# Performance work log

Hardware: AMD Instinct MI355X
Metric: run time of the kernel (lower is better)

## Reference

```python
import jax, jax.numpy as jnp
import numpy as np

N, E = 50000, 800000
IN_C, HID_C, OUT_C = 64, 64, 32
K, T = 2, 2  # num_stacks, num_layers (shared_weights=True)


def setup_inputs() -> dict:
    key = jax.random.key(0)
    ks = jax.random.split(key, 11)
    p = lambda k, shape, fan: jax.random.normal(k, shape, jnp.float32) / np.sqrt(fan)
    return {
        "x": jax.random.normal(ks[0], (N, IN_C), jnp.float32),
        "edge_index": jax.random.randint(ks[1], (2, E), 0, N, jnp.int32),
        # ARMAConv 1: in_c -> hid_c
        "init_w1": p(ks[2], (K, IN_C, HID_C), IN_C),
        "w1": p(ks[3], (1, K, HID_C, HID_C), HID_C),
        "root_w1": p(ks[4], (1, K, IN_C, HID_C), IN_C),
        "b1": 0.01 * jax.random.normal(ks[5], (1, K, 1, HID_C), jnp.float32),
        # ARMAConv 2: hid_c -> out_c
        "init_w2": p(ks[6], (K, HID_C, OUT_C), HID_C),
        "w2": p(ks[7], (1, K, OUT_C, OUT_C), OUT_C),
        "root_w2": p(ks[8], (1, K, HID_C, OUT_C), HID_C),
        "b2": 0.01 * jax.random.normal(ks[9], (1, K, 1, OUT_C), jnp.float32),
    }


def _gcn_norm(src, dst, num_nodes):
    # PyG gcn_norm with add_self_loops=False, edge_weight = 1
    deg = jax.ops.segment_sum(jnp.ones(src.shape[0], jnp.float32), dst,
                              num_segments=num_nodes)
    dinv = jnp.where(deg > 0, deg ** -0.5, 0.0)
    return dinv[src] * dinv[dst]  # [E]


def _arma_conv(x, src, dst, norm, init_w, w, root_w, b, num_nodes):
    # x: [N, F_in]; shared weights across layers, act=ReLU, eval mode (no dropout)
    root = jnp.einsum('nf,kfg->nkg', x, root_w[0]) + b[0, :, 0, :]  # [N,K,Fout]
    out = x
    for t in range(T):
        if t == 0:
            out = jnp.einsum('nf,kfg->nkg', out, init_w)        # [N,K,Fout]
        else:
            out = jnp.einsum('nkf,kfg->nkg', out, w[0])          # [N,K,Fout]
        msg = out[src] * norm[:, None, None]                      # [E,K,Fout]
        out = jax.ops.segment_sum(msg, dst, num_segments=num_nodes)
        out = jax.nn.relu(out + root)
    return out.mean(axis=1)  # mean over stacks -> [N, Fout]


def reference(x, edge_index, init_w1, w1, root_w1, b1, init_w2, w2, root_w2, b2):
    src, dst = edge_index[0], edge_index[1]
    norm = _gcn_norm(src, dst, N)
    h = jax.nn.relu(_arma_conv(x, src, dst, norm, init_w1, w1, root_w1, b1, N))
    # F.dropout is identity in eval mode
    return _arma_conv(h, src, dst, norm, init_w2, w2, root_w2, b2, N)
```

## Files before the change

kernel.cpp:

```cpp
#include <hip/hip_runtime.h>
#include <cstdint>
#include <cstddef>


#define NN 50000
#define EE 800000
#define NG (NN / 4)
#define NCHUNK ((NN + 255) / 256)

__device__ __forceinline__ float rl(float v, int l) {
  return __int_as_float(__builtin_amdgcn_readlane(__float_as_int(v), l));
}

__device__ __forceinline__ float slotb(const float4& a, int i, int c) {
  int sl = i * 16 + (c >> 2);
  switch (c & 3) {
    case 0: return rl(a.x, sl);
    case 1: return rl(a.y, sl);
    case 2: return rl(a.z, sl);
    default: return rl(a.w, sl);
  }
}


__global__ __launch_bounds__(256) void k_degree(const int* __restrict__ dst,
                                                int* __restrict__ deg) {
  int i = blockIdx.x * 256 + threadIdx.x;
  if (i < EE) atomicAdd(&deg[dst[i]], 1);
}

__global__ __launch_bounds__(256) void k_part(const int* __restrict__ deg,
                                              int* __restrict__ partial) {
  int i = blockIdx.x * 256 + threadIdx.x;
  int v = (i < NN) ? deg[i] : 0;
#pragma unroll
  for (int off = 1; off < 64; off <<= 1) v += __shfl_xor(v, off);
  __shared__ int wsum[4];
  if ((threadIdx.x & 63) == 0) wsum[threadIdx.x >> 6] = v;
  __syncthreads();
  if (threadIdx.x == 0) partial[blockIdx.x] = wsum[0] + wsum[1] + wsum[2] + wsum[3];
}

__global__ __launch_bounds__(256) void k_scanp(const int* __restrict__ partial,
                                               int* __restrict__ chunkbase) {
  __shared__ int sc[256];
  int t = threadIdx.x;
  int v = (t < NCHUNK) ? partial[t] : 0;
  sc[t] = v;
  __syncthreads();
  for (int off = 1; off < 256; off <<= 1) {
    int u = (t >= off) ? sc[t - off] : 0;
    __syncthreads();
    sc[t] += u;
    __syncthreads();
  }
  if (t < NCHUNK) chunkbase[t] = sc[t] - v;
}

__global__ __launch_bounds__(256) void k_rows(const int* __restrict__ deg,
                                              const int* __restrict__ chunkbase,
                                              int* __restrict__ rowstart,
                                              float* __restrict__ dinv,
                                              int* __restrict__ cursor) {
  __shared__ int sc[256];
  int t = threadIdx.x;
  int i = blockIdx.x * 256 + t;
  int d = (i < NN) ? deg[i] : 0;
  sc[t] = d;
  __syncthreads();
  for (int off = 1; off < 256; off <<= 1) {
    int u = (t >= off) ? sc[t - off] : 0;
    __syncthreads();
    sc[t] += u;
    __syncthreads();
  }
  if (i < NN) {
    rowstart[i] = chunkbase[blockIdx.x] + sc[t] - d;
    dinv[i] = (d > 0) ? rsqrtf((float)d) : 0.f;
    cursor[i] = 0;
  }
  if (blockIdx.x == 0 && t == 0) rowstart[NN] = EE;
}

__global__ __launch_bounds__(256) void k_fill(const int* __restrict__ src,
                                              const int* __restrict__ dst,
                                              const int* __restrict__ rowstart,
                                              int* __restrict__ cursor,
                                              int* __restrict__ csr) {
  int i = blockIdx.x * 256 + threadIdx.x;
  if (i < EE) {
    int d = dst[i];
    int pos = rowstart[d] + atomicAdd(&cursor[d], 1);
    csr[pos] = src[i];
  }
}

#define GATHER_SETUP(base)                                  \
  int n = (base) + es;                                      \
  int j = rowstart[n];                                      \
  int end = rowstart[n + 1];                                \
  int dg = end - j;                                         \
  int mtmp = max(dg, __shfl_xor(dg, 16));                   \
  mtmp = max(mtmp, __shfl_xor(mtmp, 32));                   \
  int mx = __builtin_amdgcn_readfirstlane(mtmp);


__global__ __launch_bounds__(256) void k_aggx(const float* __restrict__ x,
                                              const float* __restrict__ dinv,
                                              const int* __restrict__ rowstart,
                                              const int* __restrict__ csr,
                                              float* __restrict__ outp) {
  int lane = threadIdx.x & 63;
  int f4 = lane & 15, es = lane >> 4;
  int wg = (blockIdx.x * 256 + threadIdx.x) >> 6;
  int nwv = (gridDim.x * 256) >> 6;
  const float4* x4 = (const float4*)x;
  for (int g = wg; g < NG; g += nwv) {
    int base = g * 4;
    GATHER_SETUP(base);
    float4 a = {0.f, 0.f, 0.f, 0.f};
    for (int it = 0; it < mx; it += 2) {
      int jj0 = min(j, EE - 1), jj1 = min(j + 1, EE - 1);
      int s0 = csr[jj0], s1 = csr[jj1];
      float w0 = (j < end) ? dinv[s0] : 0.f;
      float w1 = (j + 1 < end) ? dinv[s1] : 0.f;
      float4 v0 = x4[(size_t)s0 * 16 + f4];
      float4 v1 = x4[(size_t)s1 * 16 + f4];
      a.x = fmaf(v0.x, w0, a.x); a.y = fmaf(v0.y, w0, a.y);
      a.z = fmaf(v0.z, w0, a.z); a.w = fmaf(v0.w, w0, a.w);
      a.x = fmaf(v1.x, w1, a.x); a.y = fmaf(v1.y, w1, a.y);
      a.z = fmaf(v1.z, w1, a.z); a.w = fmaf(v1.w, w1, a.w);
      j += 2;
    }
    float dn = dinv[n];
    a.x *= dn; a.y *= dn; a.z *= dn; a.w *= dn;
    ((float4*)outp)[(size_t)n * 16 + f4] = a;
  }
}


__global__ __launch_bounds__(256) void k_t0(const float* __restrict__ x,
                                            const float* __restrict__ aggxs,
                                            const float* __restrict__ initW,
                                            const float* __restrict__ rootW,
                                            const float* __restrict__ bias,
                                            const float* __restrict__ dinv,
                                            float* __restrict__ root01,
                                            float* __restrict__ s01) {
  __shared__ float Wi[8192];
  __shared__ float Wr[8192];
  for (int i = threadIdx.x; i < 8192; i += 256) { Wi[i] = initW[i]; Wr[i] = rootW[i]; }
  __syncthreads();
  int lane = threadIdx.x & 63;
  float b_0 = bias[lane], b_1 = bias[64 + lane];
  int wid = (blockIdx.x * 256 + threadIdx.x) >> 6;
  int nw = (gridDim.x * 256) >> 6;
  for (int n = wid; n < NN; n += nw) {
    float dn = dinv[n];
    float xv = x[(size_t)n * 64 + lane];
    float gv = aggxs[(size_t)n * 64 + lane];
    float r0 = b_0, r1 = b_1;
    float i0 = 0.f, i1 = 0.f;
#pragma unroll
    for (int c = 0; c < 64; c++) {
      float xc = rl(xv, c), gc = rl(gv, c);
      r0 = fmaf(xc, Wr[c * 64 + lane], r0);
      r1 = fmaf(xc, Wr[4096 + c * 64 + lane], r1);
      i0 = fmaf(gc, Wi[c * 64 + lane], i0);
      i1 = fmaf(gc, Wi[4096 + c * 64 + lane], i1);
    }
    size_t b = (size_t)n * 128 + lane;
    root01[b] = r0;
    root01[b + 64] = r1;
    s01[b] = fmaxf(i0 + r0, 0.f) * dn;
    s01[b + 64] = fmaxf(i1 + r1, 0.f) * dn;
  }
}


__global__ __launch_bounds__(256) void k_t1(const float* __restrict__ s01,
                                            const float* __restrict__ root01,
                                            const float* __restrict__ W,
                                            const float* __restrict__ dinv,
                                            const int* __restrict__ rowstart,
                                            const int* __restrict__ csr,
                                            float* __restrict__ h,
                                            float* __restrict__ hs) {
  __shared__ float Ws[8192];
  for (int i = threadIdx.x; i < 8192; i += 256) Ws[i] = W[i];
  __syncthreads();
  int lane = threadIdx.x & 63;
  int f4 = lane & 15, es = lane >> 4;
  int wg = (blockIdx.x * 256 + threadIdx.x) >> 6;
  int nwv = (gridDim.x * 256) >> 6;
  const float4* in4 = (const float4*)s01;
  for (int g = wg; g < NG; g += nwv) {
    int base = g * 4;
    GATHER_SETUP(base);
    float4 a = {0.f, 0.f, 0.f, 0.f}, b = {0.f, 0.f, 0.f, 0.f};
    for (int it = 0; it < mx; it += 2) {
      int jj0 = min(j, EE - 1), jj1 = min(j + 1, EE - 1);
      int s0 = csr[jj0], s1 = csr[jj1];
      float m0 = (j < end) ? 1.f : 0.f;
      float m1 = (j + 1 < end) ? 1.f : 0.f;
      const float4* r0 = in4 + (size_t)s0 * 32;
      const float4* r1 = in4 + (size_t)s1 * 32;
      float4 v00 = r0[f4], v01 = r0[16 + f4];
      float4 v10 = r1[f4], v11 = r1[16 + f4];
      a.x = fmaf(v00.x, m0, a.x); a.y = fmaf(v00.y, m0, a.y);
      a.z = fmaf(v00.z, m0, a.z); a.w = fmaf(v00.w, m0, a.w);
      b.x = fmaf(v01.x, m0, b.x); b.y = fmaf(v01.y, m0, b.y);
      b.z = fmaf(v01.z, m0, b.z); b.w = fmaf(v01.w, m0, b.w);
      a.x = fmaf(v10.x, m1, a.x); a.y = fmaf(v10.y, m1, a.y);
      a.z = fmaf(v10.z, m1, a.z); a.w = fmaf(v10.w, m1, a.w);
      b.x = fmaf(v11.x, m1, b.x); b.y = fmaf(v11.y, m1, b.y);
      b.z = fmaf(v11.z, m1, b.z); b.w = fmaf(v11.w, m1, b.w);
      j += 2;
    }
    float c0[4] = {0.f, 0.f, 0.f, 0.f}, c1[4] = {0.f, 0.f, 0.f, 0.f};
#pragma unroll
    for (int c = 0; c < 64; c++) {
      float w0 = Ws[c * 64 + lane];
      float w1 = Ws[4096 + c * 64 + lane];
#pragma unroll
      for (int i = 0; i < 4; i++) {
        c0[i] = fmaf(slotb(a, i, c), w0, c0[i]);
        c1[i] = fmaf(slotb(b, i, c), w1, c1[i]);
      }
    }
    float dnl = dinv[n];
#pragma unroll
    for (int i = 0; i < 4; i++) {
      float dni = rl(dnl, i * 16);
      size_t bb = (size_t)(base + i) * 128 + lane;
      float o0 = fmaxf(fmaf(dni, c0[i], root01[bb]), 0.f);
      float o1 = fmaxf(fmaf(dni, c1[i], root01[bb + 64]), 0.f);
      float hv = 0.5f * (o0 + o1);
      h[(size_t)(base + i) * 64 + lane] = hv;
      hs[(size_t)(base + i) * 64 + lane] = hv * dni;
    }
  }
}


__global__ __launch_bounds__(256) void k2_t0(const float* __restrict__ h,
                                             const float* __restrict__ hs,
                                             const float* __restrict__ initW2,
                                             const float* __restrict__ rootW2,
                                             const float* __restrict__ b2,
                                             const float* __restrict__ dinv,
                                             const int* __restrict__ rowstart,
                                             const int* __restrict__ csr,
                                             float* __restrict__ root2,
                                             float* __restrict__ s2) {
  __shared__ float Wi[4096];
  __shared__ float Wr[4096];
  for (int i = threadIdx.x; i < 4096; i += 256) { Wi[i] = initW2[i]; Wr[i] = rootW2[i]; }
  __syncthreads();
  int lane = threadIdx.x & 63;
  int f4 = lane & 15, es = lane >> 4;
  int k = lane >> 5, col = lane & 31;
  float bv = b2[lane];
  int wg = (blockIdx.x * 256 + threadIdx.x) >> 6;
  int nwv = (gridDim.x * 256) >> 6;
  const float4* in4 = (const float4*)hs;
  for (int g = wg; g < NG; g += nwv) {
    int base = g * 4;
    GATHER_SETUP(base);
    float4 a = {0.f, 0.f, 0.f, 0.f};
    for (int it = 0; it < mx; it += 2) {
      int jj0 = min(j, EE - 1), jj1 = min(j + 1, EE - 1);
      int s0 = csr[jj0], s1 = csr[jj1];
      float m0 = (j < end) ? 1.f : 0.f;
      float m1 = (j + 1 < end) ? 1.f : 0.f;
      float4 v0 = in4[(size_t)s0 * 16 + f4];
      float4 v1 = in4[(size_t)s1 * 16 + f4];
      a.x = fmaf(v0.x, m0, a.x); a.y = fmaf(v0.y, m0, a.y);
      a.z = fmaf(v0.z, m0, a.z); a.w = fmaf(v0.w, m0, a.w);
      a.x = fmaf(v1.x, m1, a.x); a.y = fmaf(v1.y, m1, a.y);
      a.z = fmaf(v1.z, m1, a.z); a.w = fmaf(v1.w, m1, a.w);
      j += 2;
    }
    float hv[4];
#pragma unroll
    for (int i = 0; i < 4; i++) hv[i] = h[(size_t)(base + i) * 64 + lane];
    float aR[4] = {bv, bv, bv, bv}, aI[4] = {0.f, 0.f, 0.f, 0.f};
#pragma unroll
    for (int c = 0; c < 64; c++) {
      float wr = Wr[k * 2048 + c * 32 + col];
      float wi = Wi[k * 2048 + c * 32 + col];
#pragma unroll
      for (int i = 0; i < 4; i++) {
        aR[i] = fmaf(rl(hv[i], c), wr, aR[i]);
        aI[i] = fmaf(slotb(a, i, c), wi, aI[i]);
      }
    }
    float dnl = dinv[n];
#pragma unroll
    for (int i = 0; i < 4; i++) {
      float dni = rl(dnl, i * 16);
      float o = fmaxf(fmaf(dni, aI[i], aR[i]), 0.f);
      root2[(size_t)(base + i) * 64 + lane] = aR[i];
      s2[(size_t)(base + i) * 64 + lane] = o * dni;
    }
  }
}


__global__ __launch_bounds__(256) void k2_t1(const float* __restrict__ s2,
                                             const float* __restrict__ root2,
                                             const float* __restrict__ W2,
                                             const float* __restrict__ dinv,
                                             const int* __restrict__ rowstart,
                                             const int* __restrict__ csr,
                                             float* __restrict__ outp) {
  __shared__ float Ws[2048];
  for (int i = threadIdx.x; i < 2048; i += 256) Ws[i] = W2[i];
  __syncthreads();
  int lane = threadIdx.x & 63;
  int f4 = lane & 15, es = lane >> 4;
  int k = lane >> 5, col = lane & 31;
  int wg = (blockIdx.x * 256 + threadIdx.x) >> 6;
  int nwv = (gridDim.x * 256) >> 6;
  const float4* in4 = (const float4*)s2;
  for (int g = wg; g < NG; g += nwv) {
    int base = g * 4;
    GATHER_SETUP(base);
    float4 a = {0.f, 0.f, 0.f, 0.f};
    for (int it = 0; it < mx; it += 2) {
      int jj0 = min(j, EE - 1), jj1 = min(j + 1, EE - 1);
      int s0 = csr[jj0], s1 = csr[jj1];
      float m0 = (j < end) ? 1.f : 0.f;
      float m1 = (j + 1 < end) ? 1.f : 0.f;
      float4 v0 = in4[(size_t)s0 * 16 + f4];
      float4 v1 = in4[(size_t)s1 * 16 + f4];
      a.x = fmaf(v0.x, m0, a.x); a.y = fmaf(v0.y, m0, a.y);
      a.z = fmaf(v0.z, m0, a.z); a.w = fmaf(v0.w, m0, a.w);
      a.x = fmaf(v1.x, m1, a.x); a.y = fmaf(v1.y, m1, a.y);
      a.z = fmaf(v1.z, m1, a.z); a.w = fmaf(v1.w, m1, a.w);
      j += 2;
    }
    float acc[4] = {0.f, 0.f, 0.f, 0.f};
#pragma unroll
    for (int c = 0; c < 32; c++) {
      float w = Ws[k * 1024 + c * 32 + col];
#pragma unroll
      for (int i = 0; i < 4; i++) {
        float p0 = slotb(a, i, c);
        float p1 = slotb(a, i, 32 + c);
        float pc = (lane < 32) ? p0 : p1;
        acc[i] = fmaf(pc, w, acc[i]);
      }
    }
    float dnl = dinv[n];
#pragma unroll
    for (int i = 0; i < 4; i++) {
      float dni = rl(dnl, i * 16);
      float o = fmaxf(fmaf(dni, acc[i], root2[(size_t)(base + i) * 64 + lane]), 0.f);
      o += __shfl_xor(o, 32);
      if (lane < 32) outp[(size_t)(base + i) * 32 + col] = 0.5f * o;
    }
  }
}


extern "C" void kernel_launch(void* const* d_in, const int* in_sizes, int n_in,
                              void* d_out, int out_size, void* d_ws, size_t ws_size,
                              hipStream_t stream) {
  const float* x = (const float*)d_in[0];
  const int* edge_index = (const int*)d_in[1];
  const float* initW1 = (const float*)d_in[2];
  const float* w1 = (const float*)d_in[3];
  const float* rootW1 = (const float*)d_in[4];
  const float* b1 = (const float*)d_in[5];
  const float* initW2 = (const float*)d_in[6];
  const float* w2 = (const float*)d_in[7];
  const float* rootW2 = (const float*)d_in[8];
  const float* b2 = (const float*)d_in[9];
  float* out = (float*)d_out;

  const int* src = edge_index;
  const int* dst = edge_index + EE;

  size_t off = 0;
  auto carve = [&](size_t bytes) {
    size_t r = off;
    off = (off + bytes + 255) & ~(size_t)255;
    return r;
  };
  char* ws = (char*)d_ws;
  int* deg = (int*)(ws + carve((size_t)NN * 4));
  int* rowstart = (int*)(ws + carve((size_t)(NN + 1) * 4));
  int* csr = (int*)(ws + carve((size_t)EE * 4));
  float* dinv = (float*)(ws + carve((size_t)NN * 4));
  int* cursor = (int*)(ws + carve((size_t)NN * 4));
  int* partial = (int*)(ws + carve(256 * 4));
  int* chunkbase = (int*)(ws + carve(256 * 4));
  float* B1 = (float*)(ws + carve((size_t)NN * 64 * 4));
  float* B2 = (float*)(ws + carve((size_t)NN * 128 * 4));
  float* B3 = (float*)(ws + carve((size_t)NN * 128 * 4));
  float* B4 = (float*)(ws + carve((size_t)NN * 64 * 4));
  (void)ws_size; (void)in_sizes; (void)n_in; (void)out_size;

  const int EB = (EE + 255) / 256;

  hipMemsetAsync(deg, 0, (size_t)NN * 4, stream);
  k_degree<<<EB, 256, 0, stream>>>(dst, deg);
  k_part<<<NCHUNK, 256, 0, stream>>>(deg, partial);
  k_scanp<<<1, 256, 0, stream>>>(partial, chunkbase);
  k_rows<<<NCHUNK, 256, 0, stream>>>(deg, chunkbase, rowstart, dinv, cursor);
  k_fill<<<EB, 256, 0, stream>>>(src, dst, rowstart, cursor, csr);

  k_aggx<<<3125, 256, 0, stream>>>(x, dinv, rowstart, csr, B1);
  k_t0<<<1024, 256, 0, stream>>>(x, B1, initW1, rootW1, b1, dinv, B2, B3);
  k_t1<<<1280, 256, 0, stream>>>(B3, B2, w1, dinv, rowstart, csr, B1, B4);
  k2_t0<<<1280, 256, 0, stream>>>(B1, B4, initW2, rootW2, b2, dinv, rowstart, csr, B2, B3);
  k2_t1<<<1536, 256, 0, stream>>>(B3, B2, w2, dinv, rowstart, csr, out);
}
```

Before: 481.1 us.

## Store gathered node features in fp16 and pre-scale x by dinv

The per-node messages gathered along edges (s01, hs, s2) are now stored as fp16 instead of fp32, which halves the bytes moved by the random-access gathers in three aggregation kernels. A new kernel pre-multiplies x by dinv, so the first aggregation no longer does a dependent dinv[src] load per edge. Out-of-range edge slots now read node 0 instead of a clamped csr entry. Half precision adds rounding error to the accumulated messages, and the pre-scale kernel adds one extra pass over x.

```diff
diff --git a/kernel.cpp b/kernel.cpp
--- a/kernel.cpp
+++ b/kernel.cpp
@@ -1,4 +1,5 @@
 #include <hip/hip_runtime.h>
+#include <hip/hip_fp16.h>
 #include <cstdint>
 #include <cstddef>
 
@@ -20,6 +21,19 @@
     case 2: return rl(a.z, sl);
     default: return rl(a.w, sl);
   }
+}
+
+__device__ __forceinline__ void addh4(float4& a, uint2 q, float m) {
+  __half2 h0 = __builtin_bit_cast(__half2, q.x);
+  __half2 h1 = __builtin_bit_cast(__half2, q.y);
+  float2 f0 = __half22float2(h0);
+  float2 f1 = __half22float2(h1);
+  a.x = fmaf(f0.x, m, a.x); a.y = fmaf(f0.y, m, a.y);
+  a.z = fmaf(f1.x, m, a.z); a.w = fmaf(f1.y, m, a.w);
+}
+
+__device__ __forceinline__ unsigned short f2h(float v) {
+  return __builtin_bit_cast(unsigned short, __float2half(v));
 }
 
 
@@ -95,6 +109,20 @@
   }
 }
 
+
+__global__ __launch_bounds__(256) void k_xd(const float* __restrict__ x,
+                                            const float* __restrict__ dinv,
+                                            float* __restrict__ xd) {
+  int i = blockIdx.x * 256 + threadIdx.x;
+  if (i < NN * 16) {
+    int n = i >> 4;
+    float d = dinv[n];
+    float4 v = ((const float4*)x)[i];
+    v.x *= d; v.y *= d; v.z *= d; v.w *= d;
+    ((float4*)xd)[i] = v;
+  }
+}
+
 #define GATHER_SETUP(base)                                  \
   int n = (base) + es;                                      \
   int j = rowstart[n];                                      \
@@ -104,8 +132,14 @@
   mtmp = max(mtmp, __shfl_xor(mtmp, 32));                   \
   int mx = __builtin_amdgcn_readfirstlane(mtmp);
 
-
-__global__ __launch_bounds__(256) void k_aggx(const float* __restrict__ x,
+#define EDGE2                                               \
+  int s0 = (j < end) ? csr[min(j, EE - 1)] : 0;             \
+  int s1 = (j + 1 < end) ? csr[min(j + 1, EE - 1)] : 0;     \
+  float m0 = (j < end) ? 1.f : 0.f;                         \
+  float m1 = (j + 1 < end) ? 1.f : 0.f;
+
+
+__global__ __launch_bounds__(256) void k_aggx(const float* __restrict__ xd,
                                               const float* __restrict__ dinv,
                                               const int* __restrict__ rowstart,
                                               const int* __restrict__ csr,
@@ -114,22 +148,19 @@
   int f4 = lane & 15, es = lane >> 4;
   int wg = (blockIdx.x * 256 + threadIdx.x) >> 6;
   int nwv = (gridDim.x * 256) >> 6;
-  const float4* x4 = (const float4*)x;
+  const float4* x4 = (const float4*)xd;
   for (int g = wg; g < NG; g += nwv) {
     int base = g * 4;
     GATHER_SETUP(base);
     float4 a = {0.f, 0.f, 0.f, 0.f};
     for (int it = 0; it < mx; it += 2) {
-      int jj0 = min(j, EE - 1), jj1 = min(j + 1, EE - 1);
-      int s0 = csr[jj0], s1 = csr[jj1];
-      float w0 = (j < end) ? dinv[s0] : 0.f;
-      float w1 = (j + 1 < end) ? dinv[s1] : 0.f;
+      EDGE2;
       float4 v0 = x4[(size_t)s0 * 16 + f4];
       float4 v1 = x4[(size_t)s1 * 16 + f4];
-      a.x = fmaf(v0.x, w0, a.x); a.y = fmaf(v0.y, w0, a.y);
-      a.z = fmaf(v0.z, w0, a.z); a.w = fmaf(v0.w, w0, a.w);
-      a.x = fmaf(v1.x, w1, a.x); a.y = fmaf(v1.y, w1, a.y);
-      a.z = fmaf(v1.z, w1, a.z); a.w = fmaf(v1.w, w1, a.w);
+      a.x = fmaf(v0.x, m0, a.x); a.y = fmaf(v0.y, m0, a.y);
+      a.z = fmaf(v0.z, m0, a.z); a.w = fmaf(v0.w, m0, a.w);
+      a.x = fmaf(v1.x, m1, a.x); a.y = fmaf(v1.y, m1, a.y);
+      a.z = fmaf(v1.z, m1, a.z); a.w = fmaf(v1.w, m1, a.w);
       j += 2;
     }
     float dn = dinv[n];
@@ -146,7 +177,7 @@
                                             const float* __restrict__ bias,
                                             const float* __restrict__ dinv,
                                             float* __restrict__ root01,
-                                            float* __restrict__ s01) {
+                                            unsigned short* __restrict__ s01h) {
   __shared__ float Wi[8192];
   __shared__ float Wr[8192];
   for (int i = threadIdx.x; i < 8192; i += 256) { Wi[i] = initW[i]; Wr[i] = rootW[i]; }
@@ -172,20 +203,20 @@
     size_t b = (size_t)n * 128 + lane;
     root01[b] = r0;
     root01[b + 64] = r1;
-    s01[b] = fmaxf(i0 + r0, 0.f) * dn;
-    s01[b + 64] = fmaxf(i1 + r1, 0.f) * dn;
-  }
-}
-
-
-__global__ __launch_bounds__(256) void k_t1(const float* __restrict__ s01,
+    s01h[b] = f2h(fmaxf(i0 + r0, 0.f) * dn);
+    s01h[b + 64] = f2h(fmaxf(i1 + r1, 0.f) * dn);
+  }
+}
+
+
+__global__ __launch_bounds__(256) void k_t1(const unsigned short* __restrict__ s01h,
                                             const float* __restrict__ root01,
                                             const float* __restrict__ W,
                                             const float* __restrict__ dinv,
                                             const int* __restrict__ rowstart,
                                             const int* __restrict__ csr,
                                             float* __restrict__ h,
-                                            float* __restrict__ hs) {
+                                            unsigned short* __restrict__ hsh) {
   __shared__ float Ws[8192];
   for (int i = threadIdx.x; i < 8192; i += 256) Ws[i] = W[i];
   __syncthreads();
@@ -193,28 +224,18 @@
   int f4 = lane & 15, es = lane >> 4;
   int wg = (blockIdx.x * 256 + threadIdx.x) >> 6;
   int nwv = (gridDim.x * 256) >> 6;
-  const float4* in4 = (const float4*)s01;
   for (int g = wg; g < NG; g += nwv) {
     int base = g * 4;
     GATHER_SETUP(base);
     float4 a = {0.f, 0.f, 0.f, 0.f}, b = {0.f, 0.f, 0.f, 0.f};
     for (int it = 0; it < mx; it += 2) {
-      int jj0 = min(j, EE - 1), jj1 = min(j + 1, EE - 1);
-      int s0 = csr[jj0], s1 = csr[jj1];
-      float m0 = (j < end) ? 1.f : 0.f;
-      float m1 = (j + 1 < end) ? 1.f : 0.f;
-      const float4* r0 = in4 + (size_t)s0 * 32;
-      const float4* r1 = in4 + (size_t)s1 * 32;
-      float4 v00 = r0[f4], v01 = r0[16 + f4];
-      float4 v10 = r1[f4], v11 = r1[16 + f4];
-      a.x = fmaf(v00.x, m0, a.x); a.y = fmaf(v00.y, m0, a.y);
-      a.z = fmaf(v00.z, m0, a.z); a.w = fmaf(v00.w, m0, a.w);
-      b.x = fmaf(v01.x, m0, b.x); b.y = fmaf(v01.y, m0, b.y);
-      b.z = fmaf(v01.z, m0, b.z); b.w = fmaf(v01.w, m0, b.w);
-      a.x = fmaf(v10.x, m1, a.x); a.y = fmaf(v10.y, m1, a.y);
-      a.z = fmaf(v10.z, m1, a.z); a.w = fmaf(v10.w, m1, a.w);
-      b.x = fmaf(v11.x, m1, b.x); b.y = fmaf(v11.y, m1, b.y);
-      b.z = fmaf(v11.z, m1, b.z); b.w = fmaf(v11.w, m1, b.w);
+      EDGE2;
+      const uint2* r0 = (const uint2*)(s01h + (size_t)s0 * 128);
+      const uint2* r1 = (const uint2*)(s01h + (size_t)s1 * 128);
+      uint2 q00 = r0[f4], q01 = r0[16 + f4];
+      uint2 q10 = r1[f4], q11 = r1[16 + f4];
+      addh4(a, q00, m0); addh4(b, q01, m0);
+      addh4(a, q10, m1); addh4(b, q11, m1);
       j += 2;
     }
     float c0[4] = {0.f, 0.f, 0.f, 0.f}, c1[4] = {0.f, 0.f, 0.f, 0.f};
@@ -237,14 +258,14 @@
       float o1 = fmaxf(fmaf(dni, c1[i], root01[bb + 64]), 0.f);
       float hv = 0.5f * (o0 + o1);
       h[(size_t)(base + i) * 64 + lane] = hv;
-      hs[(size_t)(base + i) * 64 + lane] = hv * dni;
+      hsh[(size_t)(base + i) * 64 + lane] = f2h(hv * dni);
     }
   }
 }
 
 
 __global__ __launch_bounds__(256) void k2_t0(const float* __restrict__ h,
-                                             const float* __restrict__ hs,
+                                             const unsigned short* __restrict__ hsh,
                                              const float* __restrict__ initW2,
                                              const float* __restrict__ rootW2,
                                              const float* __restrict__ b2,
@@ -252,7 +273,7 @@
                                              const int* __restrict__ rowstart,
                                              const int* __restrict__ csr,
                                              float* __restrict__ root2,
-                                             float* __restrict__ s2) {
+                                             unsigned short* __restrict__ s2h) {
   __shared__ float Wi[4096];
   __shared__ float Wr[4096];
   for (int i = threadIdx.x; i < 4096; i += 256) { Wi[i] = initW2[i]; Wr[i] = rootW2[i]; }
@@ -263,22 +284,16 @@
   float bv = b2[lane];
   int wg = (blockIdx.x * 256 + threadIdx.x) >> 6;
   int nwv = (gridDim.x * 256) >> 6;
-  const float4* in4 = (const float4*)hs;
   for (int g = wg; g < NG; g += nwv) {
     int base = g * 4;
     GATHER_SETUP(base);
     float4 a = {0.f, 0.f, 0.f, 0.f};
     for (int it = 0; it < mx; it += 2) {
-      int jj0 = min(j, EE - 1), jj1 = min(j + 1, EE - 1);
-      int s0 = csr[jj0], s1 = csr[jj1];
-      float m0 = (j < end) ? 1.f : 0.f;
-      float m1 = (j + 1 < end) ? 1.f : 0.f;
-      float4 v0 = in4[(size_t)s0 * 16 + f4];
-      float4 v1 = in4[(size_t)s1 * 16 + f4];
-      a.x = fmaf(v0.x, m0, a.x); a.y = fmaf(v0.y, m0, a.y);
-      a.z = fmaf(v0.z, m0, a.z); a.w = fmaf(v0.w, m0, a.w);
-      a.x = fmaf(v1.x, m1, a.x); a.y = fmaf(v1.y, m1, a.y);
-      a.z = fmaf(v1.z, m1, a.z); a.w = fmaf(v1.w, m1, a.w);
+      EDGE2;
+      uint2 q0 = ((const uint2*)(hsh + (size_t)s0 * 64))[f4];
+      uint2 q1 = ((const uint2*)(hsh + (size_t)s1 * 64))[f4];
+      addh4(a, q0, m0);
+      addh4(a, q1, m1);
       j += 2;
     }
     float hv[4];
@@ -301,13 +316,13 @@
       float dni = rl(dnl, i * 16);
       float o = fmaxf(fmaf(dni, aI[i], aR[i]), 0.f);
       root2[(size_t)(base + i) * 64 + lane] = aR[i];
-      s2[(size_t)(base + i) * 64 + lane] = o * dni;
-    }
-  }
-}
-
-
-__global__ __launch_bounds__(256) void k2_t1(const float* __restrict__ s2,
+      s2h[(size_t)(base + i) * 64 + lane] = f2h(o * dni);
+    }
+  }
+}
+
+
+__global__ __launch_bounds__(256) void k2_t1(const unsigned short* __restrict__ s2h,
                                              const float* __restrict__ root2,
                                              const float* __restrict__ W2,
                                              const float* __restrict__ dinv,
@@ -322,22 +337,16 @@
   int k = lane >> 5, col = lane & 31;
   int wg = (blockIdx.x * 256 + threadIdx.x) >> 6;
   int nwv = (gridDim.x * 256) >> 6;
-  const float4* in4 = (const float4*)s2;
   for (int g = wg; g < NG; g += nwv) {
     int base = g * 4;
     GATHER_SETUP(base);
     float4 a = {0.f, 0.f, 0.f, 0.f};
     for (int it = 0; it < mx; it += 2) {
-      int jj0 = min(j, EE - 1), jj1 = min(j + 1, EE - 1);
-      int s0 = csr[jj0], s1 = csr[jj1];
-      float m0 = (j < end) ? 1.f : 0.f;
-      float m1 = (j + 1 < end) ? 1.f : 0.f;
-      float4 v0 = in4[(size_t)s0 * 16 + f4];
-      float4 v1 = in4[(size_t)s1 * 16 + f4];
-      a.x = fmaf(v0.x, m0, a.x); a.y = fmaf(v0.y, m0, a.y);
-      a.z = fmaf(v0.z, m0, a.z); a.w = fmaf(v0.w, m0, a.w);
-      a.x = fmaf(v1.x, m1, a.x); a.y = fmaf(v1.y, m1, a.y);
-      a.z = fmaf(v1.z, m1, a.z); a.w = fmaf(v1.w, m1, a.w);
+      EDGE2;
+      uint2 q0 = ((const uint2*)(s2h + (size_t)s0 * 64))[f4];
+      uint2 q1 = ((const uint2*)(s2h + (size_t)s1 * 64))[f4];
+      addh4(a, q0, m0);
+      addh4(a, q1, m1);
       j += 2;
     }
     float acc[4] = {0.f, 0.f, 0.f, 0.f};
@@ -396,10 +405,11 @@
   int* cursor = (int*)(ws + carve((size_t)NN * 4));
   int* partial = (int*)(ws + carve(256 * 4));
   int* chunkbase = (int*)(ws + carve(256 * 4));
+  float* Bxd = (float*)(ws + carve((size_t)NN * 64 * 4));
   float* B1 = (float*)(ws + carve((size_t)NN * 64 * 4));
   float* B2 = (float*)(ws + carve((size_t)NN * 128 * 4));
-  float* B3 = (float*)(ws + carve((size_t)NN * 128 * 4));
-  float* B4 = (float*)(ws + carve((size_t)NN * 64 * 4));
+  unsigned short* H1 = (unsigned short*)(ws + carve((size_t)NN * 128 * 2));
+  unsigned short* H2 = (unsigned short*)(ws + carve((size_t)NN * 64 * 2));
   (void)ws_size; (void)in_sizes; (void)n_in; (void)out_size;
 
   const int EB = (EE + 255) / 256;
@@ -411,9 +421,10 @@
   k_rows<<<NCHUNK, 256, 0, stream>>>(deg, chunkbase, rowstart, dinv, cursor);
   k_fill<<<EB, 256, 0, stream>>>(src, dst, rowstart, cursor, csr);
 
-  k_aggx<<<3125, 256, 0, stream>>>(x, dinv, rowstart, csr, B1);
-  k_t0<<<1024, 256, 0, stream>>>(x, B1, initW1, rootW1, b1, dinv, B2, B3);
-  k_t1<<<1280, 256, 0, stream>>>(B3, B2, w1, dinv, rowstart, csr, B1, B4);
-  k2_t0<<<1280, 256, 0, stream>>>(B1, B4, initW2, rootW2, b2, dinv, rowstart, csr, B2, B3);
-  k2_t1<<<1536, 256, 0, stream>>>(B3, B2, w2, dinv, rowstart, csr, out);
-}
+  k_xd<<<(NN * 16 + 255) / 256, 256, 0, stream>>>(x, dinv, Bxd);
+  k_aggx<<<3125, 256, 0, stream>>>(Bxd, dinv, rowstart, csr, B1);
+  k_t0<<<1024, 256, 0, stream>>>(x, B1, initW1, rootW1, b1, dinv, B2, H1);
+  k_t1<<<1280, 256, 0, stream>>>(H1, B2, w1, dinv, rowstart, csr, B1, H2);
+  k2_t0<<<1280, 256, 0, stream>>>(B1, H2, initW2, rootW2, b2, dinv, rowstart, csr, B2, H1);
+  k2_t1<<<1536, 256, 0, stream>>>(H1, B2, w2, dinv, rowstart, csr, out);
+}
```

Result: slower. 497.3 us (+3.4%).
